# Kernel optimization log

Measured on AMD Instinct MI355X. Metric: run time of the kernel, lower is better.

The kernel has to match this reference:

```python
import jax, jax.numpy as jnp
import numpy as np

N_NODES = 100000
N_EDGES = 1600000
IN_CH, HID_CH, OUT_CH = 128, 128, 64
N_GRAPHS = 64


def gcn_conv(x, src, dst, W, b, n_nodes):
    """PyG-style GCNConv: self-loops already included in (src, dst).
    out_i = b + sum_j norm_ij * (x_j @ W), norm_ij = deg_i^-1/2 * deg_j^-1/2."""
    xw = x @ W  # [N, out]
    deg = jax.ops.segment_sum(jnp.ones_like(dst, dtype=xw.dtype), dst,
                              num_segments=n_nodes)  # [N]
    dinv = jnp.where(deg > 0, jax.lax.rsqrt(jnp.maximum(deg, 1e-12)), 0.0)
    norm = dinv[src] * dinv[dst]  # [E]
    msg = xw[src] * norm[:, None]  # gather + scale  [E, out]
    out = jax.ops.segment_sum(msg, dst, num_segments=n_nodes)  # scatter-add
    return out + b


def global_mean_pool(x, batch, n_graphs):
    s = jax.ops.segment_sum(x, batch, num_segments=n_graphs)
    cnt = jax.ops.segment_sum(jnp.ones((x.shape[0],), x.dtype), batch,
                              num_segments=n_graphs)
    return s / jnp.maximum(cnt, 1.0)[:, None]


def setup_inputs() -> dict:
    key = jax.random.key(0)
    ks = jax.random.split(key, 9)
    x = jax.random.normal(ks[0], (N_NODES, IN_CH), dtype=jnp.float32)
    edge_index = jax.random.randint(ks[1], (2, N_EDGES), 0, N_NODES, dtype=jnp.int64)
    batch = jnp.sort(jax.random.randint(ks[2], (N_NODES,), 0, N_GRAPHS, dtype=jnp.int64))
    # Glorot-ish params
    s1 = 1.0 / np.sqrt(IN_CH)
    s2 = 1.0 / np.sqrt(HID_CH)
    W1 = jax.random.normal(ks[3], (IN_CH, HID_CH), jnp.float32) * s1
    b1 = jnp.zeros((HID_CH,), jnp.float32)
    W2 = jax.random.normal(ks[4], (HID_CH, HID_CH), jnp.float32) * s2
    b2 = jnp.zeros((HID_CH,), jnp.float32)
    Wl = jax.random.normal(ks[5], (HID_CH, OUT_CH), jnp.float32) * s2
    bl = jax.random.normal(ks[6], (OUT_CH,), jnp.float32) * 0.01
    return {"x": x, "edge_index": edge_index, "batch": batch,
            "W1": W1, "b1": b1, "W2": W2, "b2": b2, "Wl": Wl, "bl": bl}


def reference(x, edge_index, batch, W1, b1, W2, b2, Wl, bl):
    n = x.shape[0]
    loop = jnp.arange(n, dtype=edge_index.dtype)
    src = jnp.concatenate([edge_index[0], loop])  # add self-loops
    dst = jnp.concatenate([edge_index[1], loop])
    h = jax.nn.relu(gcn_conv(x, src, dst, W1, b1, n))
    h = jax.nn.relu(gcn_conv(h, src, dst, W2, b2, n))
    g = global_mean_pool(h, batch, N_GRAPHS)  # [B, hid]
    return g @ Wl + bl  # [B, out]
```

## Files before the change

### kernel.cpp

```cpp
#include <hip/hip_runtime.h>

#define N_NODESC 100000
#define N_EDGESC 1600000
#define CH 128
#define NG 64
#define OC 64

#define GST_BLKS 391
#define MFMA_BLKS 1563
#define PAD_STRIDE 64
#define SENTINEL N_NODESC

#define BIN_SHIFT 9
#define BIN_W 512
#define NBINS 196
#define BIN_CAP 16384
#define BIN1_BLKS 391
#define E_PER_BIN1 4096

typedef __attribute__((ext_vector_type(8))) short short8;
typedef __attribute__((ext_vector_type(4))) float f32x4;

__device__ __forceinline__ unsigned short f2b_u(float f) {
    union { float f; unsigned int u; } x; x.f = f;
    unsigned int u = x.u;
    return (unsigned short)((u + 0x7fffu + ((u >> 16) & 1u)) >> 16);
}

#define WSTR 136
template<int AFP>
__device__ __forceinline__ void mfma_compute(int blk, int t, const void* __restrict__ Ap,
                                             signed char* __restrict__ Oq,
                                             float* __restrict__ osc,
                                             const unsigned short* WsT) {
    int wave = t >> 6, lane = t & 63;
    int quad = lane >> 4, l16 = lane & 15;
    int arow = blk * 64 + wave * 16 + l16;
    bool rowok = arow < N_NODESC;
    f32x4 acc[8] = {};
#pragma unroll
    for (int c = 0; c < 4; ++c) {
        int koff = c * 32 + quad * 8;
        short8 a;
        if (AFP) {
            const float* A = (const float*)Ap;
            float4 f0 = make_float4(0, 0, 0, 0), f1 = make_float4(0, 0, 0, 0);
            if (rowok) {
                f0 = *(const float4*)(A + (size_t)arow * 128 + koff);
                f1 = *(const float4*)(A + (size_t)arow * 128 + koff + 4);
            }
            a[0] = (short)f2b_u(f0.x); a[1] = (short)f2b_u(f0.y);
            a[2] = (short)f2b_u(f0.z); a[3] = (short)f2b_u(f0.w);
            a[4] = (short)f2b_u(f1.x); a[5] = (short)f2b_u(f1.y);
            a[6] = (short)f2b_u(f1.z); a[7] = (short)f2b_u(f1.w);
        } else {
            const unsigned short* A = (const unsigned short*)Ap;
            if (rowok) a = *(const short8*)(A + (size_t)arow * 128 + koff);
            else       a = (short8)(short)0;
        }
#pragma unroll
        for (int tt = 0; tt < 8; ++tt) {
            short8 b = *(const short8*)&WsT[(tt * 16 + l16) * WSTR + koff];
            acc[tt] = __builtin_amdgcn_mfma_f32_16x16x32_bf16(a, b, acc[tt], 0, 0, 0);
        }
    }
    int orow0 = blk * 64 + wave * 16 + quad * 4;
#pragma unroll
    for (int r = 0; r < 4; ++r) {
        int g = orow0 + r;
        float m = 0.f;
#pragma unroll
        for (int tt = 0; tt < 8; ++tt) m = fmaxf(m, fabsf(acc[tt][r]));
        m = fmaxf(m, __shfl_xor(m, 1));
        m = fmaxf(m, __shfl_xor(m, 2));
        m = fmaxf(m, __shfl_xor(m, 4));
        m = fmaxf(m, __shfl_xor(m, 8));
        float inv = m > 0.f ? 127.f / m : 0.f;
        if (g < N_NODESC) {
#pragma unroll
            for (int tt = 0; tt < 8; ++tt)
                Oq[(size_t)g * 128 + tt * 16 + l16] = (signed char)(int)rintf(acc[tt][r] * inv);
            if (l16 == 0) osc[g] = m * (1.f / 127.f);
        }
    }
}

__global__ __launch_bounds__(256) void k_pre(const int* __restrict__ ei,
                                             const int* __restrict__ batch,
                                             const float* __restrict__ W1,
                                             const float* __restrict__ W2,
                                             int* __restrict__ cursor,
                                             unsigned int* __restrict__ binbuf,
                                             unsigned short* __restrict__ Wt1,
                                             unsigned short* __restrict__ Wt2,
                                             int* __restrict__ gstart,
                                             float* __restrict__ xsc) {
    __shared__ int hist[NBINS];
    int b = blockIdx.x, t = threadIdx.x;
    if (b < BIN1_BLKS) {
        for (int i = t; i < NBINS; i += 256) hist[i] = 0;
        __syncthreads();
        int e0 = b * E_PER_BIN1;
#pragma unroll 4
        for (int i = 0; i < E_PER_BIN1 / 256; ++i) {
            int e = e0 + i * 256 + t;
            if (e < N_EDGESC) atomicAdd(&hist[ei[N_EDGESC + e] >> BIN_SHIFT], 1);
        }
        __syncthreads();
        for (int i = t; i < NBINS; i += 256) {
            int c = hist[i];
            hist[i] = c ? atomicAdd(&cursor[i], c) : 0;
        }
        __syncthreads();
#pragma unroll 4
        for (int i = 0; i < E_PER_BIN1 / 256; ++i) {
            int e = e0 + i * 256 + t;
            if (e < N_EDGESC) {
                int d = ei[N_EDGESC + e];
                int s = ei[e];
                int bin = d >> BIN_SHIFT;
                int off = atomicAdd(&hist[bin], 1);
                binbuf[(size_t)bin * BIN_CAP + off] =
                    ((unsigned int)(d & (BIN_W - 1)) << 17) | (unsigned int)s;
            }
        }
    } else if (b < BIN1_BLKS + 64) {
        int i = (b - BIN1_BLKS) * 256 + t;
        int k = i >> 7, c = i & 127;
        Wt1[c * 128 + k] = f2b_u(W1[k * 128 + c]);
    } else if (b < BIN1_BLKS + 128) {
        int i = (b - BIN1_BLKS - 64) * 256 + t;
        int k = i >> 7, c = i & 127;
        Wt2[c * 128 + k] = f2b_u(W2[k * 128 + c]);
    } else {
        int i = (b - BIN1_BLKS - 128) * 256 + t;
        if (i >= N_NODESC) {
            if (i == N_NODESC) xsc[SENTINEL] = 0.f;
            return;
        }
        int bb = batch[i];
        int bp = (i == 0) ? -1 : batch[i - 1];
        for (int g = bp + 1; g <= bb; ++g) gstart[g] = i;
        if (i == N_NODESC - 1)
            for (int g = bb + 1; g <= NG; ++g) gstart[g] = N_NODESC;
    }
}

__global__ __launch_bounds__(256) void k_main(const float* __restrict__ x,
                                              const unsigned short* __restrict__ Wt1,
                                              signed char* __restrict__ xwq,
                                              float* __restrict__ xsc,
                                              const int* __restrict__ cursor,
                                              const unsigned int* __restrict__ binbuf,
                                              int* __restrict__ deg,
                                              float* __restrict__ dinvt,
                                              int* __restrict__ pad) {
    __shared__ unsigned short WsT[128 * WSTR];
    int t = threadIdx.x;
    if (blockIdx.x < NBINS) {
        int bin = blockIdx.x;
        if (bin == 0 && t == 0) dinvt[SENTINEL] = 0.f;
        int* ldeg = (int*)WsT;
        for (int i = t; i < BIN_W; i += 256) ldeg[i] = 0;
        __syncthreads();
        int n = cursor[bin];
        size_t base = (size_t)bin * BIN_CAP;
        for (int i = t; i < n; i += 256) {
            unsigned int rec = binbuf[base + i];
            int dl = rec >> 17;
            int s = rec & 0x1FFFF;
            int slot = atomicAdd(&ldeg[dl], 1) & (PAD_STRIDE - 1);
            pad[(size_t)((bin << BIN_SHIFT) + dl) * PAD_STRIDE + slot] = s;
        }
        __syncthreads();
        for (int i = t; i < BIN_W; i += 256) {
            int node = (bin << BIN_SHIFT) + i;
            if (node < N_NODESC) {
                int dg = ldeg[i];
                if (dg > PAD_STRIDE) dg = PAD_STRIDE;
                deg[node] = dg;
                dinvt[node] = rsqrtf((float)(dg + 1));
                int r8 = (dg + 7) & ~7;
                for (int j = dg; j < r8; ++j)
                    pad[(size_t)node * PAD_STRIDE + j] = SENTINEL;
            }
        }
    } else {
        int blk = blockIdx.x - NBINS;
        const uint4* wsrc = (const uint4*)Wt1;
        for (int idx = t; idx < 2048; idx += 256) {
            int row = idx >> 4, sub = idx & 15;
            *((uint4*)&WsT[row * WSTR] + sub) = wsrc[row * 16 + sub];
        }
        __syncthreads();
        mfma_compute<1>(blk, t, x, xwq, xsc, WsT);
    }
}

__global__ __launch_bounds__(256) void k_mfma2(const unsigned short* __restrict__ A,
                                               const unsigned short* __restrict__ Wt,
                                               signed char* __restrict__ Oq,
                                               float* __restrict__ osc) {
    __shared__ unsigned short WsT[128 * WSTR];
    int t = threadIdx.x;
    {
        const uint4* wsrc = (const uint4*)Wt;
        for (int idx = t; idx < 2048; idx += 256) {
            int row = idx >> 4, sub = idx & 15;
            *((uint4*)&WsT[row * WSTR] + sub) = wsrc[row * 16 + sub];
        }
    }
    __syncthreads();
    mfma_compute<0>(blockIdx.x, t, A, Oq, osc, WsT);
}

__global__ __launch_bounds__(256) void k_wsc(const float* __restrict__ dinvt,
                                             const float* __restrict__ xsc,
                                             float* __restrict__ wsc) {
    int i = blockIdx.x * 256 + threadIdx.x;
    if (i <= N_NODESC) wsc[i] = dinvt[i] * xsc[i];
}

__device__ __forceinline__ void accq(float* acc, unsigned int lo, unsigned int hi, float wk) {
    acc[0] += wk * (float)((int)(lo << 24) >> 24);
    acc[1] += wk * (float)((int)(lo << 16) >> 24);
    acc[2] += wk * (float)((int)(lo <<  8) >> 24);
    acc[3] += wk * (float)((int)lo >> 24);
    acc[4] += wk * (float)((int)(hi << 24) >> 24);
    acc[5] += wk * (float)((int)(hi << 16) >> 24);
    acc[6] += wk * (float)((int)(hi <<  8) >> 24);
    acc[7] += wk * (float)((int)hi >> 24);
}

__device__ __forceinline__ void gather_pair(const signed char* __restrict__ xwq,
                                            const float* __restrict__ wsc,
                                            const int* __restrict__ pad,
                                            int nA, int nB, int nbA, int nbB,
                                            int l16, float* accA, float* accB) {
    const int4* prA = (const int4*)&pad[nA * PAD_STRIDE];
    const int4* prB = (const int4*)&pad[nB * PAD_STRIDE];
    int nmax = nbA > nbB ? nbA : nbB;
    for (int kb = 0; kb < nmax; ++kb) {
        int4 a0 = prA[kb * 2], a1 = prA[kb * 2 + 1];
        int4 b0 = prB[kb * 2], b1 = prB[kb * 2 + 1];
        bool inA = kb < nbA, inB = kb < nbB;
        int s[16];
        s[0]  = inA ? a0.x : SENTINEL; s[1]  = inA ? a0.y : SENTINEL;
        s[2]  = inA ? a0.z : SENTINEL; s[3]  = inA ? a0.w : SENTINEL;
        s[4]  = inA ? a1.x : SENTINEL; s[5]  = inA ? a1.y : SENTINEL;
        s[6]  = inA ? a1.z : SENTINEL; s[7]  = inA ? a1.w : SENTINEL;
        s[8]  = inB ? b0.x : SENTINEL; s[9]  = inB ? b0.y : SENTINEL;
        s[10] = inB ? b0.z : SENTINEL; s[11] = inB ? b0.w : SENTINEL;
        s[12] = inB ? b1.x : SENTINEL; s[13] = inB ? b1.y : SENTINEL;
        s[14] = inB ? b1.z : SENTINEL; s[15] = inB ? b1.w : SENTINEL;
        float w[16];
        uint2 v[16];
#pragma unroll
        for (int k = 0; k < 16; ++k) {
            w[k] = wsc[s[k]];
            v[k] = *(const uint2*)&xwq[(size_t)(unsigned int)s[k] * 128 + l16 * 8];
        }
#pragma unroll
        for (int k = 0; k < 8; ++k) accq(accA, v[k].x, v[k].y, w[k]);
#pragma unroll
        for (int k = 0; k < 8; ++k) accq(accB, v[8 + k].x, v[8 + k].y, w[8 + k]);
    }
}

__global__ __launch_bounds__(256) void k_gather1(const signed char* __restrict__ xwq,
                                                 const float* __restrict__ wsc,
                                                 const int* __restrict__ deg,
                                                 const float* __restrict__ dinvt,
                                                 const int* __restrict__ pad,
                                                 const float* __restrict__ bias,
                                                 unsigned int* __restrict__ outp) {
    int t = threadIdx.x;
    int lane = t & 63, w = t >> 6;
    int g = lane >> 4, l16 = lane & 15;
    int nA = blockIdx.x * 32 + w * 8 + g * 2;
    int nB = nA + 1;
    int dgA = deg[nA], dgB = deg[nB];
    float wnA = dinvt[nA], wnB = dinvt[nB];
    float wsA = wsc[nA], wsB = wsc[nB];
    uint2 vsA = *(const uint2*)&xwq[(size_t)(unsigned int)nA * 128 + l16 * 8];
    uint2 vsB = *(const uint2*)&xwq[(size_t)(unsigned int)nB * 128 + l16 * 8];
    float accA[8] = {0.f, 0.f, 0.f, 0.f, 0.f, 0.f, 0.f, 0.f};
    float accB[8] = {0.f, 0.f, 0.f, 0.f, 0.f, 0.f, 0.f, 0.f};
    accq(accA, vsA.x, vsA.y, wsA);
    accq(accB, vsB.x, vsB.y, wsB);
    gather_pair(xwq, wsc, pad, nA, nB, (dgA + 7) >> 3, (dgB + 7) >> 3, l16, accA, accB);
    float4 bA = *(const float4*)&bias[l16 * 8];
    float4 bB = *(const float4*)&bias[l16 * 8 + 4];
    float oA[8], oB[8];
    oA[0] = fmaxf(bA.x + wnA * accA[0], 0.f); oA[1] = fmaxf(bA.y + wnA * accA[1], 0.f);
    oA[2] = fmaxf(bA.z + wnA * accA[2], 0.f); oA[3] = fmaxf(bA.w + wnA * accA[3], 0.f);
    oA[4] = fmaxf(bB.x + wnA * accA[4], 0.f); oA[5] = fmaxf(bB.y + wnA * accA[5], 0.f);
    oA[6] = fmaxf(bB.z + wnA * accA[6], 0.f); oA[7] = fmaxf(bB.w + wnA * accA[7], 0.f);
    oB[0] = fmaxf(bA.x + wnB * accB[0], 0.f); oB[1] = fmaxf(bA.y + wnB * accB[1], 0.f);
    oB[2] = fmaxf(bA.z + wnB * accB[2], 0.f); oB[3] = fmaxf(bA.w + wnB * accB[3], 0.f);
    oB[4] = fmaxf(bB.x + wnB * accB[4], 0.f); oB[5] = fmaxf(bB.y + wnB * accB[5], 0.f);
    oB[6] = fmaxf(bB.z + wnB * accB[6], 0.f); oB[7] = fmaxf(bB.w + wnB * accB[7], 0.f);
    uint4 ovA, ovB;
    ovA.x = ((unsigned int)f2b_u(oA[1]) << 16) | (unsigned int)f2b_u(oA[0]);
    ovA.y = ((unsigned int)f2b_u(oA[3]) << 16) | (unsigned int)f2b_u(oA[2]);
    ovA.z = ((unsigned int)f2b_u(oA[5]) << 16) | (unsigned int)f2b_u(oA[4]);
    ovA.w = ((unsigned int)f2b_u(oA[7]) << 16) | (unsigned int)f2b_u(oA[6]);
    ovB.x = ((unsigned int)f2b_u(oB[1]) << 16) | (unsigned int)f2b_u(oB[0]);
    ovB.y = ((unsigned int)f2b_u(oB[3]) << 16) | (unsigned int)f2b_u(oB[2]);
    ovB.z = ((unsigned int)f2b_u(oB[5]) << 16) | (unsigned int)f2b_u(oB[4]);
    ovB.w = ((unsigned int)f2b_u(oB[7]) << 16) | (unsigned int)f2b_u(oB[6]);
    *(uint4*)&outp[(unsigned int)nA * 64 + l16 * 4] = ovA;
    *(uint4*)&outp[(unsigned int)nB * 64 + l16 * 4] = ovB;
}

__global__ __launch_bounds__(256) void k_gather_pool(const signed char* __restrict__ xwq,
                                                     const float* __restrict__ wsc,
                                                     const int* __restrict__ deg,
                                                     const float* __restrict__ dinvt,
                                                     const int* __restrict__ pad,
                                                     const float* __restrict__ bias,
                                                     const int* __restrict__ batch,
                                                     float* __restrict__ gpart) {
    __shared__ float lds[4 * 128];
    int t = threadIdx.x, w = t >> 6, lane = t & 63;
    int g = lane >> 4, l16 = lane & 15;
    int base = blockIdx.x * 32;
    int nA = base + w * 8 + g * 2;
    int nB = nA + 1;
    int dgA = deg[nA], dgB = deg[nB];
    float wnA = dinvt[nA], wnB = dinvt[nB];
    float wsA = wsc[nA], wsB = wsc[nB];
    uint2 vsA = *(const uint2*)&xwq[(size_t)(unsigned int)nA * 128 + l16 * 8];
    uint2 vsB = *(const uint2*)&xwq[(size_t)(unsigned int)nB * 128 + l16 * 8];
    float accA[8] = {0.f, 0.f, 0.f, 0.f, 0.f, 0.f, 0.f, 0.f};
    float accB[8] = {0.f, 0.f, 0.f, 0.f, 0.f, 0.f, 0.f, 0.f};
    accq(accA, vsA.x, vsA.y, wsA);
    accq(accB, vsB.x, vsB.y, wsB);
    gather_pair(xwq, wsc, pad, nA, nB, (dgA + 7) >> 3, (dgB + 7) >> 3, l16, accA, accB);
    float4 bA = *(const float4*)&bias[l16 * 8];
    float4 bB = *(const float4*)&bias[l16 * 8 + 4];
    float oA[8], oB[8];
    oA[0] = fmaxf(bA.x + wnA * accA[0], 0.f); oA[1] = fmaxf(bA.y + wnA * accA[1], 0.f);
    oA[2] = fmaxf(bA.z + wnA * accA[2], 0.f); oA[3] = fmaxf(bA.w + wnA * accA[3], 0.f);
    oA[4] = fmaxf(bB.x + wnA * accA[4], 0.f); oA[5] = fmaxf(bB.y + wnA * accA[5], 0.f);
    oA[6] = fmaxf(bB.z + wnA * accA[6], 0.f); oA[7] = fmaxf(bB.w + wnA * accA[7], 0.f);
    oB[0] = fmaxf(bA.x + wnB * accB[0], 0.f); oB[1] = fmaxf(bA.y + wnB * accB[1], 0.f);
    oB[2] = fmaxf(bA.z + wnB * accB[2], 0.f); oB[3] = fmaxf(bA.w + wnB * accB[3], 0.f);
    oB[4] = fmaxf(bB.x + wnB * accB[4], 0.f); oB[5] = fmaxf(bB.y + wnB * accB[5], 0.f);
    oB[6] = fmaxf(bB.z + wnB * accB[6], 0.f); oB[7] = fmaxf(bB.w + wnB * accB[7], 0.f);
    bool fast = batch[base] == batch[base + 31];
    if (fast) {
#pragma unroll
        for (int j = 0; j < 8; ++j) {
            float v = oA[j] + oB[j];
            v += __shfl_xor(v, 16);
            v += __shfl_xor(v, 32);
            oA[j] = v;
        }
        if (lane < 16) {
#pragma unroll
            for (int j = 0; j < 8; ++j) lds[w * 128 + l16 * 8 + j] = oA[j];
        }
        __syncthreads();
        if (t < 128) {
            float v = lds[t] + lds[128 + t] + lds[256 + t] + lds[384 + t];
            atomicAdd(&gpart[batch[base] * 128 + t], v);
        }
    } else {
        int gA = batch[nA], gB = batch[nB];
#pragma unroll
        for (int j = 0; j < 8; ++j) {
            atomicAdd(&gpart[gA * 128 + l16 * 8 + j], oA[j]);
            atomicAdd(&gpart[gB * 128 + l16 * 8 + j], oB[j]);
        }
    }
}

__global__ void k_final(const float* __restrict__ gpart, const int* __restrict__ gstart,
                        const float* __restrict__ Wl, const float* __restrict__ bl,
                        float* __restrict__ out) {
    __shared__ float gs[128];
    int b = blockIdx.x;
    int o = threadIdx.x;
    gs[o] = gpart[b * 128 + o];
    gs[o + 64] = gpart[b * 128 + 64 + o];
    __syncthreads();
    int cnt = gstart[b + 1] - gstart[b];
    float sc = 1.f / (float)(cnt > 0 ? cnt : 1);
    float sum = 0.f;
    for (int k = 0; k < 128; ++k) sum += gs[k] * Wl[k * 64 + o];
    out[b * 64 + o] = bl[o] + sc * sum;
}

extern "C" void kernel_launch(void* const* d_in, const int* in_sizes, int n_in,
                              void* d_out, int out_size, void* d_ws, size_t ws_size,
                              hipStream_t stream) {
    const float* x    = (const float*)d_in[0];
    const int*   ei   = (const int*)d_in[1];
    const int*   batch= (const int*)d_in[2];
    const float* W1   = (const float*)d_in[3];
    const float* b1   = (const float*)d_in[4];
    const float* W2   = (const float*)d_in[5];
    const float* b2   = (const float*)d_in[6];
    const float* Wl   = (const float*)d_in[7];
    const float* bl   = (const float*)d_in[8];
    float* out = (float*)d_out;

    char* ws = (char*)d_ws;
    signed char* xwq = (signed char*)ws; ws += (size_t)(N_NODESC + 1) * CH;
    unsigned short* h_b = (unsigned short*)ws; ws += (size_t)N_NODESC * CH * 2;
    unsigned short* Wt1 = (unsigned short*)ws; ws += (size_t)CH * CH * 2;
    unsigned short* Wt2 = (unsigned short*)ws; ws += (size_t)CH * CH * 2;
    int*   cursor = (int*)ws;   ws += (size_t)NBINS * 4;
    float* gpart  = (float*)ws; ws += (size_t)NG * CH * 4;
    int*   deg    = (int*)ws;   ws += (size_t)N_NODESC * 4;
    float* dinvt  = (float*)ws; ws += (size_t)(N_NODESC + 4) * 4;
    float* xsc    = (float*)ws; ws += (size_t)(N_NODESC + 4) * 4;
    float* wsc    = (float*)ws; ws += (size_t)(N_NODESC + 4) * 4;
    int*   pad    = (int*)ws;   ws += (size_t)N_NODESC * PAD_STRIDE * 4;
    unsigned int* binbuf = (unsigned int*)ws; ws += (size_t)NBINS * BIN_CAP * 4;
    int*   gstart = (int*)ws;   ws += (NG + 8) * 4;

    hipMemsetAsync(cursor, 0, (size_t)NBINS * 4 + (size_t)NG * CH * 4, stream);

    k_pre<<<BIN1_BLKS + 128 + GST_BLKS, 256, 0, stream>>>(ei, batch, W1, W2,
        cursor, binbuf, Wt1, Wt2, gstart, xsc);
    k_main<<<NBINS + MFMA_BLKS, 256, 0, stream>>>(x, Wt1, xwq, xsc, cursor, binbuf,
                                                  deg, dinvt, pad);
    k_wsc<<<GST_BLKS, 256, 0, stream>>>(dinvt, xsc, wsc);

    k_gather1<<<N_NODESC / 32, 256, 0, stream>>>(xwq, wsc, deg, dinvt, pad, b1,
                                                 (unsigned int*)h_b);
    k_mfma2<<<MFMA_BLKS, 256, 0, stream>>>(h_b, Wt2, xwq, xsc);
    k_wsc<<<GST_BLKS, 256, 0, stream>>>(dinvt, xsc, wsc);
    k_gather_pool<<<N_NODESC / 32, 256, 0, stream>>>(xwq, wsc, deg, dinvt, pad, b2,
                                                     batch, gpart);

    k_final<<<NG, 64, 0, stream>>>(gpart, gstart, Wl, bl, out);
}
```

Baseline: 300.4 us.

## Fold wsc scaling into producers and move first GEMM into preprocessing kernel

The layer-1 MFMA GEMM moves into k_pre, where each block converts W1 to bf16 transposed in shared memory, so the separate Wt1 pass goes away. Bin stage 2 becomes its own kernel that also writes wsc = dinv * xscale. The second GEMM writes the dinv-scaled row scale directly. Both k_wsc launches are removed. The cost is that every GEMM block redundantly converts W1 from fp32 with strided LDS writes, and k_pre now carries heavy shared memory for all of its blocks.

```diff
diff --git a/kernel.cpp b/kernel.cpp
--- a/kernel.cpp
+++ b/kernel.cpp
@@ -18,6 +18,8 @@
 #define BIN1_BLKS 391
 #define E_PER_BIN1 4096
 
+#define K0_BLKS (BIN1_BLKS + 64 + GST_BLKS + MFMA_BLKS)
+
 typedef __attribute__((ext_vector_type(8))) short short8;
 typedef __attribute__((ext_vector_type(4))) float f32x4;
 
@@ -28,10 +30,11 @@
 }
 
 #define WSTR 136
-template<int AFP>
+template<int AFP, int DM>
 __device__ __forceinline__ void mfma_compute(int blk, int t, const void* __restrict__ Ap,
                                              signed char* __restrict__ Oq,
                                              float* __restrict__ osc,
+                                             const float* __restrict__ dmul,
                                              const unsigned short* WsT) {
     int wave = t >> 6, lane = t & 63;
     int quad = lane >> 4, l16 = lane & 15;
@@ -80,7 +83,10 @@
 #pragma unroll
             for (int tt = 0; tt < 8; ++tt)
                 Oq[(size_t)g * 128 + tt * 16 + l16] = (signed char)(int)rintf(acc[tt][r] * inv);
-            if (l16 == 0) osc[g] = m * (1.f / 127.f);
+            if (l16 == 0) {
+                float s = m * (1.f / 127.f);
+                osc[g] = DM ? dmul[g] * s : s;
+            }
         }
     }
 }
@@ -91,13 +97,15 @@
                                              const float* __restrict__ W2,
                                              int* __restrict__ cursor,
                                              unsigned int* __restrict__ binbuf,
-                                             unsigned short* __restrict__ Wt1,
                                              unsigned short* __restrict__ Wt2,
                                              int* __restrict__ gstart,
-                                             float* __restrict__ xsc) {
-    __shared__ int hist[NBINS];
+                                             float* __restrict__ xsc,
+                                             const float* __restrict__ x,
+                                             signed char* __restrict__ xwq) {
+    __shared__ unsigned short WsT[128 * WSTR];
     int b = blockIdx.x, t = threadIdx.x;
     if (b < BIN1_BLKS) {
+        int* hist = (int*)WsT;
         for (int i = t; i < NBINS; i += 256) hist[i] = 0;
         __syncthreads();
         int e0 = b * E_PER_BIN1;
@@ -127,13 +135,9 @@
     } else if (b < BIN1_BLKS + 64) {
         int i = (b - BIN1_BLKS) * 256 + t;
         int k = i >> 7, c = i & 127;
-        Wt1[c * 128 + k] = f2b_u(W1[k * 128 + c]);
-    } else if (b < BIN1_BLKS + 128) {
+        Wt2[c * 128 + k] = f2b_u(W2[k * 128 + c]);
+    } else if (b < BIN1_BLKS + 64 + GST_BLKS) {
         int i = (b - BIN1_BLKS - 64) * 256 + t;
-        int k = i >> 7, c = i & 127;
-        Wt2[c * 128 + k] = f2b_u(W2[k * 128 + c]);
-    } else {
-        int i = (b - BIN1_BLKS - 128) * 256 + t;
         if (i >= N_NODESC) {
             if (i == N_NODESC) xsc[SENTINEL] = 0.f;
             return;
@@ -143,64 +147,60 @@
         for (int g = bp + 1; g <= bb; ++g) gstart[g] = i;
         if (i == N_NODESC - 1)
             for (int g = bb + 1; g <= NG; ++g) gstart[g] = N_NODESC;
-    }
-}
-
-__global__ __launch_bounds__(256) void k_main(const float* __restrict__ x,
-                                              const unsigned short* __restrict__ Wt1,
-                                              signed char* __restrict__ xwq,
-                                              float* __restrict__ xsc,
-                                              const int* __restrict__ cursor,
+    } else {
+        int blk = b - (BIN1_BLKS + 64 + GST_BLKS);
+        for (int idx = t; idx < 16384; idx += 256) {
+            int k = idx >> 7, c = idx & 127;
+            WsT[c * WSTR + k] = f2b_u(W1[idx]);
+        }
+        __syncthreads();
+        mfma_compute<1, 0>(blk, t, x, xwq, xsc, nullptr, WsT);
+    }
+}
+
+__global__ __launch_bounds__(256) void k_bin2(const int* __restrict__ cursor,
                                               const unsigned int* __restrict__ binbuf,
+                                              const float* __restrict__ xsc,
                                               int* __restrict__ deg,
                                               float* __restrict__ dinvt,
+                                              float* __restrict__ wsc,
                                               int* __restrict__ pad) {
-    __shared__ unsigned short WsT[128 * WSTR];
-    int t = threadIdx.x;
-    if (blockIdx.x < NBINS) {
-        int bin = blockIdx.x;
-        if (bin == 0 && t == 0) dinvt[SENTINEL] = 0.f;
-        int* ldeg = (int*)WsT;
-        for (int i = t; i < BIN_W; i += 256) ldeg[i] = 0;
-        __syncthreads();
-        int n = cursor[bin];
-        size_t base = (size_t)bin * BIN_CAP;
-        for (int i = t; i < n; i += 256) {
-            unsigned int rec = binbuf[base + i];
-            int dl = rec >> 17;
-            int s = rec & 0x1FFFF;
-            int slot = atomicAdd(&ldeg[dl], 1) & (PAD_STRIDE - 1);
-            pad[(size_t)((bin << BIN_SHIFT) + dl) * PAD_STRIDE + slot] = s;
-        }
-        __syncthreads();
-        for (int i = t; i < BIN_W; i += 256) {
-            int node = (bin << BIN_SHIFT) + i;
-            if (node < N_NODESC) {
-                int dg = ldeg[i];
-                if (dg > PAD_STRIDE) dg = PAD_STRIDE;
-                deg[node] = dg;
-                dinvt[node] = rsqrtf((float)(dg + 1));
-                int r8 = (dg + 7) & ~7;
-                for (int j = dg; j < r8; ++j)
-                    pad[(size_t)node * PAD_STRIDE + j] = SENTINEL;
-            }
-        }
-    } else {
-        int blk = blockIdx.x - NBINS;
-        const uint4* wsrc = (const uint4*)Wt1;
-        for (int idx = t; idx < 2048; idx += 256) {
-            int row = idx >> 4, sub = idx & 15;
-            *((uint4*)&WsT[row * WSTR] + sub) = wsrc[row * 16 + sub];
-        }
-        __syncthreads();
-        mfma_compute<1>(blk, t, x, xwq, xsc, WsT);
+    __shared__ int ldeg[BIN_W];
+    int bin = blockIdx.x, t = threadIdx.x;
+    if (bin == 0 && t == 0) { dinvt[SENTINEL] = 0.f; wsc[SENTINEL] = 0.f; }
+    for (int i = t; i < BIN_W; i += 256) ldeg[i] = 0;
+    __syncthreads();
+    int n = cursor[bin];
+    size_t base = (size_t)bin * BIN_CAP;
+    for (int i = t; i < n; i += 256) {
+        unsigned int rec = binbuf[base + i];
+        int dl = rec >> 17;
+        int s = rec & 0x1FFFF;
+        int slot = atomicAdd(&ldeg[dl], 1) & (PAD_STRIDE - 1);
+        pad[(size_t)((bin << BIN_SHIFT) + dl) * PAD_STRIDE + slot] = s;
+    }
+    __syncthreads();
+    for (int i = t; i < BIN_W; i += 256) {
+        int node = (bin << BIN_SHIFT) + i;
+        if (node < N_NODESC) {
+            int dg = ldeg[i];
+            if (dg > PAD_STRIDE) dg = PAD_STRIDE;
+            deg[node] = dg;
+            float dv = rsqrtf((float)(dg + 1));
+            dinvt[node] = dv;
+            wsc[node] = dv * xsc[node];
+            int r8 = (dg + 7) & ~7;
+            for (int j = dg; j < r8; ++j)
+                pad[(size_t)node * PAD_STRIDE + j] = SENTINEL;
+        }
     }
 }
 
 __global__ __launch_bounds__(256) void k_mfma2(const unsigned short* __restrict__ A,
                                                const unsigned short* __restrict__ Wt,
                                                signed char* __restrict__ Oq,
-                                               float* __restrict__ osc) {
+                                               float* __restrict__ wsc,
+                                               const float* __restrict__ dinvt) {
     __shared__ unsigned short WsT[128 * WSTR];
     int t = threadIdx.x;
     {
@@ -211,14 +211,7 @@
         }
     }
     __syncthreads();
-    mfma_compute<0>(blockIdx.x, t, A, Oq, osc, WsT);
-}
-
-__global__ __launch_bounds__(256) void k_wsc(const float* __restrict__ dinvt,
-                                             const float* __restrict__ xsc,
-                                             float* __restrict__ wsc) {
-    int i = blockIdx.x * 256 + threadIdx.x;
-    if (i <= N_NODESC) wsc[i] = dinvt[i] * xsc[i];
+    mfma_compute<0, 1>(blockIdx.x, t, A, Oq, wsc, dinvt, WsT);
 }
 
 __device__ __forceinline__ void accq(float* acc, unsigned int lo, unsigned int hi, float wk) {
@@ -409,7 +402,6 @@
     char* ws = (char*)d_ws;
     signed char* xwq = (signed char*)ws; ws += (size_t)(N_NODESC + 1) * CH;
     unsigned short* h_b = (unsigned short*)ws; ws += (size_t)N_NODESC * CH * 2;
-    unsigned short* Wt1 = (unsigned short*)ws; ws += (size_t)CH * CH * 2;
     unsigned short* Wt2 = (unsigned short*)ws; ws += (size_t)CH * CH * 2;
     int*   cursor = (int*)ws;   ws += (size_t)NBINS * 4;
     float* gpart  = (float*)ws; ws += (size_t)NG * CH * 4;
@@ -423,16 +415,13 @@
 
     hipMemsetAsync(cursor, 0, (size_t)NBINS * 4 + (size_t)NG * CH * 4, stream);
 
-    k_pre<<<BIN1_BLKS + 128 + GST_BLKS, 256, 0, stream>>>(ei, batch, W1, W2,
-        cursor, binbuf, Wt1, Wt2, gstart, xsc);
-    k_main<<<NBINS + MFMA_BLKS, 256, 0, stream>>>(x, Wt1, xwq, xsc, cursor, binbuf,
-                                                  deg, dinvt, pad);
-    k_wsc<<<GST_BLKS, 256, 0, stream>>>(dinvt, xsc, wsc);
+    k_pre<<<K0_BLKS, 256, 0, stream>>>(ei, batch, W1, W2, cursor, binbuf,
+                                       Wt2, gstart, xsc, x, xwq);
+    k_bin2<<<NBINS, 256, 0, stream>>>(cursor, binbuf, xsc, deg, dinvt, wsc, pad);
 
     k_gather1<<<N_NODESC / 32, 256, 0, stream>>>(xwq, wsc, deg, dinvt, pad, b1,
                                                  (unsigned int*)h_b);
-    k_mfma2<<<MFMA_BLKS, 256, 0, stream>>>(h_b, Wt2, xwq, xsc);
-    k_wsc<<<GST_BLKS, 256, 0, stream>>>(dinvt, xsc, wsc);
+    k_mfma2<<<MFMA_BLKS, 256, 0, stream>>>(h_b, Wt2, xwq, wsc, dinvt);
     k_gather_pool<<<N_NODESC / 32, 256, 0, stream>>>(xwq, wsc, deg, dinvt, pad, b2,
                                                      batch, gpart);
 
```

New measurement: 294.6 us. About the same (-1.9%).
